# Kernel optimization log

Hardware: AMD Instinct MI355X
Metric: run time of the kernel (lower is better)

The kernel has to match this reference:

```python
import jax, jax.numpy as jnp
import numpy as np

NUM_BUCKETS = 32
MAX_DISTANCE = 128


def _rel_bucket(relative_position):
    """T5 relative-position bucketing, bidirectional=False (causal)."""
    n = jnp.maximum(-relative_position, 0)  # distance looking back
    max_exact = NUM_BUCKETS // 2
    is_small = n < max_exact
    nf = jnp.maximum(n.astype(jnp.float32), 1.0)
    val_large = max_exact + (
        jnp.log(nf / max_exact) / np.log(MAX_DISTANCE / max_exact)
        * (NUM_BUCKETS - max_exact)
    ).astype(jnp.int32)
    val_large = jnp.minimum(val_large, NUM_BUCKETS - 1)
    return jnp.where(is_small, n, val_large)


def setup_inputs() -> dict:
    key = jax.random.key(0)
    B, L, E, H, D, F = 4, 2048, 1024, 16, 64, 4096
    ks = jax.random.split(key, 8)
    inputs = jax.random.normal(ks[0], (B, L, E), jnp.float32)
    wq = jax.random.normal(ks[1], (E, H, D), jnp.float32) * (E ** -0.5)
    wk = jax.random.normal(ks[2], (E, H, D), jnp.float32) * (E ** -0.5)
    wv = jax.random.normal(ks[3], (E, H, D), jnp.float32) * (E ** -0.5)
    wo = jax.random.normal(ks[4], (H, D, E), jnp.float32) * ((H * D) ** -0.5)
    wi = jax.random.normal(ks[5], (E, F), jnp.float32) * (E ** -0.5)
    wmo = jax.random.normal(ks[6], (F, E), jnp.float32) * (F ** -0.5)
    rel_emb = jax.random.normal(ks[7], (NUM_BUCKETS, H), jnp.float32)
    decoder_mask = jnp.tril(jnp.ones((L, L), bool))[None, None]  # causal [1,1,L,L]
    return dict(inputs=inputs, wq=wq, wk=wk, wv=wv, wo=wo, wi=wi,
                wmo=wmo, rel_emb=rel_emb, decoder_mask=decoder_mask)


def reference(inputs, wq, wk, wv, wo, wi, wmo, rel_emb, decoder_mask):
    B, L, E = inputs.shape
    # --- T5 relative position bias: [1, H, L, L] ---
    pos = jnp.arange(L)
    rp = pos[None, :] - pos[:, None]  # memory_pos - query_pos
    bias = rel_emb[_rel_bucket(rp)]               # [L, L, H]
    bias = jnp.transpose(bias, (2, 0, 1))[None]   # [1, H, L, L]

    # NOTE: the provided source computes LayerNorm into `x` but feeds the raw
    # `inputs` (as lnx) to attention and MLP; we follow the source literally.
    lnx = inputs

    # --- self attention with additive relpos bias ---
    q = jnp.einsum('ble,ehd->blhd', lnx, wq)
    k = jnp.einsum('ble,ehd->blhd', lnx, wk)
    v = jnp.einsum('ble,ehd->blhd', lnx, wv)
    D = q.shape[-1]
    scores = jnp.einsum('bqhd,bkhd->bhqk', q, k) / jnp.sqrt(jnp.asarray(D, q.dtype))
    scores = scores + bias
    scores = jnp.where(decoder_mask, scores, jnp.finfo(scores.dtype).min)
    probs = jax.nn.softmax(scores, axis=-1)
    ctx = jnp.einsum('bhqk,bkhd->bqhd', probs, v)
    attn = jnp.einsum('bqhd,hde->bqe', ctx, wo)

    # --- parallel MLP (relu) off the same lnx ---
    mlp = jnp.einsum('blf,fe->ble', jax.nn.relu(jnp.einsum('ble,ef->blf', lnx, wi)), wmo)

    # residual sum (dropout deterministic -> no-op)
    return inputs + mlp + attn
```

## Files before the change

### kernel.cpp

```cpp
#include <hip/hip_runtime.h>
#include <stdint.h>

typedef short bf16x8 __attribute__((ext_vector_type(8)));
typedef float f32x4 __attribute__((ext_vector_type(4)));

__device__ __forceinline__ short f2bf(float f) {
  unsigned int u = __float_as_uint(f);
  u = (u + 0x7FFFu + ((u >> 16) & 1u)) >> 16;
  return (short)u;
}

__device__ __forceinline__ void gload_lds16(const void* g, void* l) {
  __builtin_amdgcn_global_load_lds((const __attribute__((address_space(1))) void*)g,
                                   (__attribute__((address_space(3))) void*)l, 16, 0, 0);
}
__device__ __forceinline__ void gload_lds4(const void* g, void* l) {
  __builtin_amdgcn_global_load_lds((const __attribute__((address_space(1))) void*)g,
                                   (__attribute__((address_space(3))) void*)l, 4, 0, 0);
}

__device__ __forceinline__ void xcd_remap(int& mIdx, int& nIdx) {
  int id = blockIdx.y * gridDim.x + blockIdx.x;
  int xcd = id & 7, local = id >> 3;
  mIdx = ((local & 7) << 3) | xcd;
  nIdx = local >> 3;
}

__global__ void prep_kernel(const float* __restrict__ inputs, const float* __restrict__ wq,
                            const float* __restrict__ wk, const float* __restrict__ wv,
                            const float* __restrict__ wi, const float* __restrict__ wo,
                            const float* __restrict__ wmo, const float* __restrict__ rel_emb,
                            short* __restrict__ x16, short* __restrict__ wcat1,
                            short* __restrict__ wcat, float* __restrict__ btab) {
  const int t = threadIdx.x;
  int id = blockIdx.x;

  if (id < 8192) {
    int i = id * 256 + t;
    float4 v = ((const float4*)inputs)[i];
    short4 o;
    o.x = f2bf(v.x); o.y = f2bf(v.y); o.z = f2bf(v.z); o.w = f2bf(v.w);
    ((short4*)x16)[i] = o;
    return;
  }
  id -= 8192;

  if (id >= 12288) {
    int i = (id - 12288) * 256 + t;
    int h = i >> 11, n = i & 2047;
    int bucket;
    if (n < 16) {
      bucket = n;
    } else {
      float tv = logf((float)n * 0.0625f) * (16.0f / 2.0794415416798357f);
      bucket = 16 + (int)tv;
      if (bucket > 31) bucket = 31;
    }
    btab[i] = rel_emb[bucket * 16 + h] * 1.4426950408889634f - 28.853900817779268f;
    return;
  }

  const float* in; short* out; int C, ldout, bx, by;
  if (id < 1024)      { in = wq;  out = wcat1;                C = 1024; ldout = 1024; int r = id;         bx = r & 31;  by = r >> 5; }
  else if (id < 2048) { in = wk;  out = wcat1 + 1024 * 1024;  C = 1024; ldout = 1024; int r = id - 1024;  bx = r & 31;  by = r >> 5; }
  else if (id < 3072) { in = wv;  out = wcat1 + 2048 * 1024;  C = 1024; ldout = 1024; int r = id - 2048;  bx = r & 31;  by = r >> 5; }
  else if (id < 7168) { in = wi;  out = wcat1 + 3072 * 1024;  C = 4096; ldout = 1024; int r = id - 3072;  bx = r & 127; by = r >> 7; }
  else if (id < 8192) { in = wo;  out = wcat;                 C = 1024; ldout = 5120; int r = id - 7168;  bx = r & 31;  by = r >> 5; }
  else                { in = wmo; out = wcat + 1024;          C = 1024; ldout = 5120; int r = id - 8192;  bx = r & 31;  by = r >> 5; }

  __shared__ float tile[32][33];
  int tx = t & 31, ty = t >> 5;
  int c0 = bx * 32, r0 = by * 32;
#pragma unroll
  for (int j = 0; j < 4; j++)
    tile[ty + j * 8][tx] = in[(size_t)(r0 + ty + j * 8) * C + c0 + tx];
  __syncthreads();
#pragma unroll
  for (int j = 0; j < 4; j++)
    out[(size_t)(c0 + ty + j * 8) * ldout + r0 + tx] = f2bf(tile[tx][ty + j * 8]);
}

__global__ void transpose_v_kernel(const short* __restrict__ qkv, short* __restrict__ vT) {
  __shared__ short tile[32][33];
  int tx = threadIdx.x & 31, ty = threadIdx.x >> 5;
  int l0 = blockIdx.x * 32, d0 = blockIdx.y * 32;
  int bh = blockIdx.z, b = bh >> 4, h = bh & 15;
#pragma unroll
  for (int j = 0; j < 4; j++)
    tile[ty + j * 8][tx] =
        qkv[(size_t)(b * 2048 + l0 + ty + j * 8) * 3072 + 2048 + h * 64 + d0 + tx];
  __syncthreads();
#pragma unroll
  for (int j = 0; j < 4; j++)
    vT[((size_t)bh * 64 + d0 + ty + j * 8) * 2048 + l0 + tx] = tile[tx][ty + j * 8];
}

__global__ __launch_bounds__(256, 3)
void gemm_qkvmlp_kernel(const short* __restrict__ A, const short* __restrict__ Bt,
                        short* __restrict__ qkv, short* __restrict__ hidden, int xoff) {
  __shared__ short lA[128 * 64];
  __shared__ short lB[128 * 64];
  const int t = threadIdx.x;
  const int w = t >> 6, lane = t & 63;
  const int q4 = lane >> 4, l15 = lane & 15;
  int mIdx, nIdx;
  xcd_remap(mIdx, nIdx);
  const int mBase = mIdx * 128, nBase = (nIdx + xoff) * 128;
  const int wm = (w >> 1) * 64, wn = (w & 1) * 64;
  const int K = 1024;

  const f32x4 fzero = {0.f, 0.f, 0.f, 0.f};
  f32x4 acc[4][4];
#pragma unroll
  for (int i = 0; i < 4; i++)
#pragma unroll
    for (int j = 0; j < 4; j++) acc[i][j] = fzero;

  for (int k0 = 0; k0 < K; k0 += 64) {
    __syncthreads();
#pragma unroll
    for (int p = 0; p < 4; p++) {
      int c = p * 256 + t;
      int row = c >> 3;
      int kc = ((c & 7) - row) & 7;
      gload_lds16(A + (size_t)(mBase + row) * K + k0 + kc * 8, lA + (size_t)(c - lane) * 8);
      gload_lds16(Bt + (size_t)(nBase + row) * K + k0 + kc * 8, lB + (size_t)(c - lane) * 8);
    }
    __syncthreads();
#pragma unroll
    for (int ks = 0; ks < 2; ks++) {
      bf16x8 af[4], bfr[4];
#pragma unroll
      for (int mi = 0; mi < 4; mi++) {
        int row = wm + mi * 16 + l15;
        af[mi] = *(const bf16x8*)&lA[row * 64 + ((ks * 4 + q4 + row) & 7) * 8];
      }
#pragma unroll
      for (int ni = 0; ni < 4; ni++) {
        int row = wn + ni * 16 + l15;
        bfr[ni] = *(const bf16x8*)&lB[row * 64 + ((ks * 4 + q4 + row) & 7) * 8];
      }
#pragma unroll
      for (int mi = 0; mi < 4; mi++)
#pragma unroll
        for (int ni = 0; ni < 4; ni++)
          acc[mi][ni] =
              __builtin_amdgcn_mfma_f32_16x16x32_bf16(af[mi], bfr[ni], acc[mi][ni], 0, 0, 0);
    }
  }

  const bool isMlp = nBase >= 3072;
  short* Cb = isMlp ? hidden : qkv;
  const int ldC = isMlp ? 4096 : 3072;
  const int ncol = isMlp ? nBase - 3072 : nBase;
#pragma unroll
  for (int mi = 0; mi < 4; mi++)
#pragma unroll
    for (int ni = 0; ni < 4; ni++) {
#pragma unroll
      for (int r = 0; r < 4; r++) {
        size_t idx = (size_t)(mBase + wm + mi * 16 + q4 * 4 + r) * ldC +
                     (ncol + wn + ni * 16 + l15);
        float v = acc[mi][ni][r];
        if (isMlp && v < 0.f) v = 0.f;
        Cb[idx] = f2bf(v);
      }
    }
}

__global__ __launch_bounds__(256, 3)
void gemm_cat_kernel(const short* __restrict__ ctx, const short* __restrict__ hidden,
                     const short* __restrict__ wcat, const float* __restrict__ resid,
                     float* __restrict__ out) {
  __shared__ short lA[128 * 64];
  __shared__ short lB[128 * 64];
  const int t = threadIdx.x;
  const int w = t >> 6, lane = t & 63;
  const int q4 = lane >> 4, l15 = lane & 15;
  int mIdx, nIdx;
  xcd_remap(mIdx, nIdx);
  const int mBase = mIdx * 128, nBase = nIdx * 128;
  const int wm = (w >> 1) * 64, wn = (w & 1) * 64;

  const f32x4 fzero = {0.f, 0.f, 0.f, 0.f};
  f32x4 acc[4][4];
#pragma unroll
  for (int i = 0; i < 4; i++)
#pragma unroll
    for (int j = 0; j < 4; j++) acc[i][j] = fzero;

  for (int k0 = 0; k0 < 5120; k0 += 64) {
    const short* Abase = (k0 < 1024) ? (ctx + k0) : (hidden + (k0 - 1024));
    const size_t lda = (k0 < 1024) ? 1024 : 4096;
    __syncthreads();
#pragma unroll
    for (int p = 0; p < 4; p++) {
      int c = p * 256 + t;
      int row = c >> 3;
      int kc = ((c & 7) - row) & 7;
      gload_lds16(Abase + (size_t)(mBase + row) * lda + kc * 8, lA + (size_t)(c - lane) * 8);
      gload_lds16(wcat + (size_t)(nBase + row) * 5120 + k0 + kc * 8,
                  lB + (size_t)(c - lane) * 8);
    }
    __syncthreads();
#pragma unroll
    for (int ks = 0; ks < 2; ks++) {
      bf16x8 af[4], bfr[4];
#pragma unroll
      for (int mi = 0; mi < 4; mi++) {
        int row = wm + mi * 16 + l15;
        af[mi] = *(const bf16x8*)&lA[row * 64 + ((ks * 4 + q4 + row) & 7) * 8];
      }
#pragma unroll
      for (int ni = 0; ni < 4; ni++) {
        int row = wn + ni * 16 + l15;
        bfr[ni] = *(const bf16x8*)&lB[row * 64 + ((ks * 4 + q4 + row) & 7) * 8];
      }
#pragma unroll
      for (int mi = 0; mi < 4; mi++)
#pragma unroll
        for (int ni = 0; ni < 4; ni++)
          acc[mi][ni] =
              __builtin_amdgcn_mfma_f32_16x16x32_bf16(af[mi], bfr[ni], acc[mi][ni], 0, 0, 0);
    }
  }

#pragma unroll
  for (int mi = 0; mi < 4; mi++)
#pragma unroll
    for (int ni = 0; ni < 4; ni++) {
#pragma unroll
      for (int r = 0; r < 4; r++) {
        size_t idx = (size_t)(mBase + wm + mi * 16 + q4 * 4 + r) * 1024 +
                     (nBase + wn + ni * 16 + l15);
        out[idx] = acc[mi][ni][r] + resid[idx];
      }
    }
}

__global__ __launch_bounds__(256, 5)
void attn_kernel(const short* __restrict__ qkv, const short* __restrict__ vT,
                 const float* __restrict__ bias_tab, short* __restrict__ ctx) {
  __shared__ short lK[64 * 64];
  __shared__ short lV[64 * 64];
  __shared__ short lP[4][16 * 64];
  __shared__ float lBias[128];

  const int t = threadIdx.x, w = t >> 6, lane = t & 63;
  const int q4 = lane >> 4, l15 = lane & 15;
  const int bh = blockIdx.x;
  const int qt = 31 - blockIdx.y;
  const int b = bh >> 4, h = bh & 15;
  const int q0 = qt * 64;
  const int ntiles = qt + 1;
  const f32x4 fzero = {0.f, 0.f, 0.f, 0.f};
  const float C1 = 0.125f * 1.4426950408889634f;

  const size_t qrow = (size_t)(b * 2048 + q0 + w * 16 + l15) * 3072 + h * 64;
  bf16x8 aq0 = *(const bf16x8*)(qkv + qrow + q4 * 8);
  bf16x8 aq1 = *(const bf16x8*)(qkv + qrow + 32 + q4 * 8);

  f32x4 vacc[4];
#pragma unroll
  for (int db = 0; db < 4; db++) vacc[db] = fzero;
  float l_part[4] = {0.f, 0.f, 0.f, 0.f};

  const float* btab = bias_tab + h * 2048;
  const int qrow0 = q0 + w * 16 + q4 * 4;
  const int bofs = w * 16 + q4 * 4 + 63 - l15;

  for (int kt = 0; kt < ntiles; kt++) {
    __syncthreads();
#pragma unroll
    for (int p = 0; p < 2; p++) {
      int c = p * 256 + t;
      int row = c >> 3;
      int kc = ((c & 7) - row) & 7;
      gload_lds16(qkv + (size_t)(b * 2048 + kt * 64 + row) * 3072 + 1024 + h * 64 + kc * 8,
                  lK + (size_t)(c - lane) * 8);
    }
#pragma unroll
    for (int p = 0; p < 2; p++) {
      int c = p * 256 + t;
      int d = c >> 3;
      int vc = ((c & 7) - d) & 7;
      gload_lds16(vT + ((size_t)bh * 64 + d) * 2048 + kt * 64 + vc * 8,
                  lV + (size_t)(c - lane) * 8);
    }
    if (w < 2) {
      int d = q0 - kt * 64 - 63 + t;
      d = d < 0 ? 0 : (d > 2047 ? 2047 : d);
      gload_lds4(btab + d, lBias + (t - lane));
    }
    __syncthreads();

    float pr[4][4];
#pragma unroll
    for (int nb = 0; nb < 4; nb++) {
      int row = nb * 16 + l15;
      bf16x8 bk0 = *(const bf16x8*)&lK[row * 64 + ((q4 + row) & 7) * 8];
      bf16x8 bk1 = *(const bf16x8*)&lK[row * 64 + ((q4 + 4 + row) & 7) * 8];
      f32x4 f = fzero;
      f = __builtin_amdgcn_mfma_f32_16x16x32_bf16(aq0, bk0, f, 0, 0, 0);
      f = __builtin_amdgcn_mfma_f32_16x16x32_bf16(aq1, bk1, f, 0, 0, 0);
      const int kcol = kt * 64 + row;
#pragma unroll
      for (int r = 0; r < 4; r++) {
        int dist = (qrow0 + r) - kcol;
        float tv = f[r] * C1 + lBias[bofs + r - nb * 16];
        float pv = __builtin_amdgcn_exp2f(tv);
        pv = (dist < 0) ? 0.f : pv;
        pr[nb][r] = pv;
        l_part[r] += pv;
      }
    }

    short* lPw = lP[w];
#pragma unroll
    for (int nb = 0; nb < 4; nb++) {
      int c = nb * 2 + (l15 >> 3);
#pragma unroll
      for (int r = 0; r < 4; r++) {
        int row = q4 * 4 + r;
        lPw[row * 64 + ((c + row) & 7) * 8 + (l15 & 7)] = f2bf(pr[nb][r]);
      }
    }

    bf16x8 ap[2];
#pragma unroll
    for (int ks2 = 0; ks2 < 2; ks2++)
      ap[ks2] = *(const bf16x8*)&lPw[l15 * 64 + ((ks2 * 4 + q4 + l15) & 7) * 8];
#pragma unroll
    for (int db = 0; db < 4; db++) {
      int row = db * 16 + l15;
#pragma unroll
      for (int ks2 = 0; ks2 < 2; ks2++) {
        bf16x8 bv = *(const bf16x8*)&lV[row * 64 + ((ks2 * 4 + q4 + row) & 7) * 8];
        vacc[db] = __builtin_amdgcn_mfma_f32_16x16x32_bf16(ap[ks2], bv, vacc[db], 0, 0, 0);
      }
    }
  }

  float inv[4];
#pragma unroll
  for (int r = 0; r < 4; r++) {
    float ps = l_part[r];
    ps += __shfl_xor(ps, 1);
    ps += __shfl_xor(ps, 2);
    ps += __shfl_xor(ps, 4);
    ps += __shfl_xor(ps, 8);
    inv[r] = 1.0f / ps;
  }
#pragma unroll
  for (int db = 0; db < 4; db++)
#pragma unroll
    for (int r = 0; r < 4; r++) {
      size_t idx = (size_t)(b * 2048 + q0 + w * 16 + q4 * 4 + r) * 1024 +
                   h * 64 + db * 16 + l15;
      ctx[idx] = f2bf(vacc[db][r] * inv[r]);
    }
}

extern "C" void kernel_launch(void* const* d_in, const int* in_sizes, int n_in,
                              void* d_out, int out_size, void* d_ws, size_t ws_size,
                              hipStream_t stream) {
  (void)in_sizes; (void)n_in; (void)out_size;
  const float* inputs  = (const float*)d_in[0];
  const float* wq      = (const float*)d_in[1];
  const float* wk      = (const float*)d_in[2];
  const float* wv      = (const float*)d_in[3];
  const float* wo      = (const float*)d_in[4];
  const float* wi      = (const float*)d_in[5];
  const float* wmo     = (const float*)d_in[6];
  const float* rel_emb = (const float*)d_in[7];
  float* out = (float*)d_out;
  char* ws = (char*)d_ws;
  const size_t MB = 1ull << 20;
  const bool big = ws_size >= 171 * MB;

  short *x16, *qkv, *hidden, *vT, *wcat1, *wcat, *ctx;
  float* btab;
  if (big) {
    x16    = (short*)(ws + 0);
    ctx    = (short*)(ws + 0);
    qkv    = (short*)(ws + 16 * MB);
    vT     = (short*)(ws + 64 * MB);
    hidden = (short*)(ws + 80 * MB);
    wcat1  = (short*)(ws + 144 * MB);
    wcat   = (short*)(ws + 158 * MB);
    btab   = (float*)(ws + 169 * MB);
  } else {
    x16    = (short*)(ws + 0);
    qkv    = (short*)(ws + 16 * MB);
    hidden = (short*)(ws + 16 * MB);
    vT     = (short*)(ws + 64 * MB);
    wcat1  = (short*)(ws + 80 * MB);
    wcat   = (short*)(ws + 94 * MB);
    btab   = (float*)(ws + 105 * MB);
    ctx    = (short*)(ws + 106 * MB);
  }

  prep_kernel<<<20608, 256, 0, stream>>>(inputs, wq, wk, wv, wi, wo, wmo, rel_emb,
                                         x16, wcat1, wcat, btab);
  if (big) {
    gemm_qkvmlp_kernel<<<dim3(56, 64), 256, 0, stream>>>(x16, wcat1, qkv, hidden, 0);
    transpose_v_kernel<<<dim3(64, 2, 64), 256, 0, stream>>>(qkv, vT);
    attn_kernel<<<dim3(64, 32), 256, 0, stream>>>(qkv, vT, btab, ctx);
  } else {
    gemm_qkvmlp_kernel<<<dim3(24, 64), 256, 0, stream>>>(x16, wcat1, qkv, hidden, 0);
    transpose_v_kernel<<<dim3(64, 2, 64), 256, 0, stream>>>(qkv, vT);
    attn_kernel<<<dim3(64, 32), 256, 0, stream>>>(qkv, vT, btab, ctx);
    gemm_qkvmlp_kernel<<<dim3(32, 64), 256, 0, stream>>>(x16, wcat1, qkv, hidden, 24);
  }
  gemm_cat_kernel<<<dim3(8, 64), 256, 0, stream>>>(ctx, hidden, wcat, inputs, out);
}
```

Baseline: 430.0 us.

## Enlarge attention query tile to 128 rows, two 16-row subtiles per wave

Each attention block now handles 128 query rows instead of 64, and each wave computes two 16-row M subtiles. Every K/V tile loaded into LDS therefore feeds twice as many MFMAs, and the grid is halved. The cost is more registers (launch bounds drop to 4 waves/SIMD), larger LDS for P, and coarser causal granularity, so the diagonal tiles do more masked work and load balance across blocks is worse. The workspace threshold also moves slightly and the launch code is reorganised.

```diff
diff --git a/kernel.cpp b/kernel.cpp
--- a/kernel.cpp
+++ b/kernel.cpp
@@ -238,36 +238,41 @@
     }
 }
 
-__global__ __launch_bounds__(256, 5)
+__global__ __launch_bounds__(256, 4)
 void attn_kernel(const short* __restrict__ qkv, const short* __restrict__ vT,
                  const float* __restrict__ bias_tab, short* __restrict__ ctx) {
   __shared__ short lK[64 * 64];
   __shared__ short lV[64 * 64];
-  __shared__ short lP[4][16 * 64];
-  __shared__ float lBias[128];
+  __shared__ short lP[4][32 * 64];
+  __shared__ float lBias[192];
 
   const int t = threadIdx.x, w = t >> 6, lane = t & 63;
   const int q4 = lane >> 4, l15 = lane & 15;
   const int bh = blockIdx.x;
-  const int qt = 31 - blockIdx.y;
+  const int qq = 15 - blockIdx.y;
   const int b = bh >> 4, h = bh & 15;
-  const int q0 = qt * 64;
-  const int ntiles = qt + 1;
+  const int q0 = qq * 128;
+  const int ntiles = 2 * qq + 2;
   const f32x4 fzero = {0.f, 0.f, 0.f, 0.f};
   const float C1 = 0.125f * 1.4426950408889634f;
 
-  const size_t qrow = (size_t)(b * 2048 + q0 + w * 16 + l15) * 3072 + h * 64;
-  bf16x8 aq0 = *(const bf16x8*)(qkv + qrow + q4 * 8);
-  bf16x8 aq1 = *(const bf16x8*)(qkv + qrow + 32 + q4 * 8);
-
-  f32x4 vacc[4];
-#pragma unroll
-  for (int db = 0; db < 4; db++) vacc[db] = fzero;
-  float l_part[4] = {0.f, 0.f, 0.f, 0.f};
+  bf16x8 aq[2][2];
+#pragma unroll
+  for (int mt = 0; mt < 2; mt++) {
+    const size_t qrow = (size_t)(b * 2048 + q0 + w * 32 + mt * 16 + l15) * 3072 + h * 64;
+    aq[mt][0] = *(const bf16x8*)(qkv + qrow + q4 * 8);
+    aq[mt][1] = *(const bf16x8*)(qkv + qrow + 32 + q4 * 8);
+  }
+
+  f32x4 vacc[2][4];
+#pragma unroll
+  for (int mt = 0; mt < 2; mt++)
+#pragma unroll
+    for (int db = 0; db < 4; db++) vacc[mt][db] = fzero;
+  float l_part[2][4] = {{0.f, 0.f, 0.f, 0.f}, {0.f, 0.f, 0.f, 0.f}};
 
   const float* btab = bias_tab + h * 2048;
-  const int qrow0 = q0 + w * 16 + q4 * 4;
-  const int bofs = w * 16 + q4 * 4 + 63 - l15;
+  const int bof = w * 32 + q4 * 4 + 63 - l15;
 
   for (int kt = 0; kt < ntiles; kt++) {
     __syncthreads();
@@ -287,78 +292,94 @@
       gload_lds16(vT + ((size_t)bh * 64 + d) * 2048 + kt * 64 + vc * 8,
                   lV + (size_t)(c - lane) * 8);
     }
-    if (w < 2) {
+    if (w < 3) {
       int d = q0 - kt * 64 - 63 + t;
       d = d < 0 ? 0 : (d > 2047 ? 2047 : d);
       gload_lds4(btab + d, lBias + (t - lane));
     }
     __syncthreads();
 
-    float pr[4][4];
+    float pr[2][4][4];
 #pragma unroll
     for (int nb = 0; nb < 4; nb++) {
       int row = nb * 16 + l15;
       bf16x8 bk0 = *(const bf16x8*)&lK[row * 64 + ((q4 + row) & 7) * 8];
       bf16x8 bk1 = *(const bf16x8*)&lK[row * 64 + ((q4 + 4 + row) & 7) * 8];
-      f32x4 f = fzero;
-      f = __builtin_amdgcn_mfma_f32_16x16x32_bf16(aq0, bk0, f, 0, 0, 0);
-      f = __builtin_amdgcn_mfma_f32_16x16x32_bf16(aq1, bk1, f, 0, 0, 0);
       const int kcol = kt * 64 + row;
 #pragma unroll
-      for (int r = 0; r < 4; r++) {
-        int dist = (qrow0 + r) - kcol;
-        float tv = f[r] * C1 + lBias[bofs + r - nb * 16];
-        float pv = __builtin_amdgcn_exp2f(tv);
-        pv = (dist < 0) ? 0.f : pv;
-        pr[nb][r] = pv;
-        l_part[r] += pv;
+      for (int mt = 0; mt < 2; mt++) {
+        f32x4 f = fzero;
+        f = __builtin_amdgcn_mfma_f32_16x16x32_bf16(aq[mt][0], bk0, f, 0, 0, 0);
+        f = __builtin_amdgcn_mfma_f32_16x16x32_bf16(aq[mt][1], bk1, f, 0, 0, 0);
+        const int qloc = w * 32 + mt * 16 + q4 * 4;
+#pragma unroll
+        for (int r = 0; r < 4; r++) {
+          int dist = (q0 + qloc + r) - kcol;
+          float tv = f[r] * C1 + lBias[bof + mt * 16 + r - nb * 16];
+          float pv = __builtin_amdgcn_exp2f(tv);
+          pv = (dist < 0) ? 0.f : pv;
+          pr[mt][nb][r] = pv;
+          l_part[mt][r] += pv;
+        }
       }
     }
 
     short* lPw = lP[w];
 #pragma unroll
-    for (int nb = 0; nb < 4; nb++) {
-      int c = nb * 2 + (l15 >> 3);
-#pragma unroll
-      for (int r = 0; r < 4; r++) {
-        int row = q4 * 4 + r;
-        lPw[row * 64 + ((c + row) & 7) * 8 + (l15 & 7)] = f2bf(pr[nb][r]);
-      }
-    }
-
-    bf16x8 ap[2];
-#pragma unroll
-    for (int ks2 = 0; ks2 < 2; ks2++)
-      ap[ks2] = *(const bf16x8*)&lPw[l15 * 64 + ((ks2 * 4 + q4 + l15) & 7) * 8];
+    for (int mt = 0; mt < 2; mt++)
+#pragma unroll
+      for (int nb = 0; nb < 4; nb++) {
+        int c = nb * 2 + (l15 >> 3);
+#pragma unroll
+        for (int r = 0; r < 4; r++) {
+          int row = mt * 16 + q4 * 4 + r;
+          lPw[row * 64 + ((c + row) & 7) * 8 + (l15 & 7)] = f2bf(pr[mt][nb][r]);
+        }
+      }
+
+    bf16x8 ap[2][2];
+#pragma unroll
+    for (int mt = 0; mt < 2; mt++) {
+      int row = mt * 16 + l15;
+#pragma unroll
+      for (int ks2 = 0; ks2 < 2; ks2++)
+        ap[mt][ks2] = *(const bf16x8*)&lPw[row * 64 + ((ks2 * 4 + q4 + row) & 7) * 8];
+    }
 #pragma unroll
     for (int db = 0; db < 4; db++) {
       int row = db * 16 + l15;
 #pragma unroll
       for (int ks2 = 0; ks2 < 2; ks2++) {
         bf16x8 bv = *(const bf16x8*)&lV[row * 64 + ((ks2 * 4 + q4 + row) & 7) * 8];
-        vacc[db] = __builtin_amdgcn_mfma_f32_16x16x32_bf16(ap[ks2], bv, vacc[db], 0, 0, 0);
-      }
-    }
-  }
-
-  float inv[4];
-#pragma unroll
-  for (int r = 0; r < 4; r++) {
-    float ps = l_part[r];
-    ps += __shfl_xor(ps, 1);
-    ps += __shfl_xor(ps, 2);
-    ps += __shfl_xor(ps, 4);
-    ps += __shfl_xor(ps, 8);
-    inv[r] = 1.0f / ps;
-  }
-#pragma unroll
-  for (int db = 0; db < 4; db++)
+#pragma unroll
+        for (int mt = 0; mt < 2; mt++)
+          vacc[mt][db] =
+              __builtin_amdgcn_mfma_f32_16x16x32_bf16(ap[mt][ks2], bv, vacc[mt][db], 0, 0, 0);
+      }
+    }
+  }
+
+#pragma unroll
+  for (int mt = 0; mt < 2; mt++) {
+    float inv[4];
 #pragma unroll
     for (int r = 0; r < 4; r++) {
-      size_t idx = (size_t)(b * 2048 + q0 + w * 16 + q4 * 4 + r) * 1024 +
-                   h * 64 + db * 16 + l15;
-      ctx[idx] = f2bf(vacc[db][r] * inv[r]);
-    }
+      float ps = l_part[mt][r];
+      ps += __shfl_xor(ps, 1);
+      ps += __shfl_xor(ps, 2);
+      ps += __shfl_xor(ps, 4);
+      ps += __shfl_xor(ps, 8);
+      inv[r] = 1.0f / ps;
+    }
+#pragma unroll
+    for (int db = 0; db < 4; db++)
+#pragma unroll
+      for (int r = 0; r < 4; r++) {
+        size_t idx = (size_t)(b * 2048 + q0 + w * 32 + mt * 16 + q4 * 4 + r) * 1024 +
+                     h * 64 + db * 16 + l15;
+        ctx[idx] = f2bf(vacc[mt][db][r] * inv[r]);
+      }
+  }
 }
 
 extern "C" void kernel_launch(void* const* d_in, const int* in_sizes, int n_in,
@@ -376,11 +397,10 @@
   float* out = (float*)d_out;
   char* ws = (char*)d_ws;
   const size_t MB = 1ull << 20;
-  const bool big = ws_size >= 171 * MB;
 
   short *x16, *qkv, *hidden, *vT, *wcat1, *wcat, *ctx;
   float* btab;
-  if (big) {
+  if (ws_size >= 170 * MB) {
     x16    = (short*)(ws + 0);
     ctx    = (short*)(ws + 0);
     qkv    = (short*)(ws + 16 * MB);
@@ -389,6 +409,12 @@
     wcat1  = (short*)(ws + 144 * MB);
     wcat   = (short*)(ws + 158 * MB);
     btab   = (float*)(ws + 169 * MB);
+
+    prep_kernel<<<20608, 256, 0, stream>>>(inputs, wq, wk, wv, wi, wo, wmo, rel_emb,
+                                           x16, wcat1, wcat, btab);
+    gemm_qkvmlp_kernel<<<dim3(56, 64), 256, 0, stream>>>(x16, wcat1, qkv, hidden, 0);
+    transpose_v_kernel<<<dim3(64, 2, 64), 256, 0, stream>>>(qkv, vT);
+    attn_kernel<<<dim3(64, 16), 256, 0, stream>>>(qkv, vT, btab, ctx);
   } else {
     x16    = (short*)(ws + 0);
     qkv    = (short*)(ws + 16 * MB);
@@ -398,18 +424,12 @@
     wcat   = (short*)(ws + 94 * MB);
     btab   = (float*)(ws + 105 * MB);
     ctx    = (short*)(ws + 106 * MB);
-  }
-
-  prep_kernel<<<20608, 256, 0, stream>>>(inputs, wq, wk, wv, wi, wo, wmo, rel_emb,
-                                         x16, wcat1, wcat, btab);
-  if (big) {
-    gemm_qkvmlp_kernel<<<dim3(56, 64), 256, 0, stream>>>(x16, wcat1, qkv, hidden, 0);
-    transpose_v_kernel<<<dim3(64, 2, 64), 256, 0, stream>>>(qkv, vT);
-    attn_kernel<<<dim3(64, 32), 256, 0, stream>>>(qkv, vT, btab, ctx);
-  } else {
+
+    prep_kernel<<<20608, 256, 0, stream>>>(inputs, wq, wk, wv, wi, wo, wmo, rel_emb,
+                                           x16, wcat1, wcat, btab);
     gemm_qkvmlp_kernel<<<dim3(24, 64), 256, 0, stream>>>(x16, wcat1, qkv, hidden, 0);
     transpose_v_kernel<<<dim3(64, 2, 64), 256, 0, stream>>>(qkv, vT);
-    attn_kernel<<<dim3(64, 32), 256, 0, stream>>>(qkv, vT, btab, ctx);
+    attn_kernel<<<dim3(64, 16), 256, 0, stream>>>(qkv, vT, btab, ctx);
     gemm_qkvmlp_kernel<<<dim3(32, 64), 256, 0, stream>>>(x16, wcat1, qkv, hidden, 24);
   }
   gemm_cat_kernel<<<dim3(8, 64), 256, 0, stream>>>(ctx, hidden, wcat, inputs, out);
```

Result: slower. 621.2 us (+44.5%).
